# Kernel optimization log

Measured on AMD Instinct MI355X. Metric: run time of the kernel, lower is better.

## Reference

```python
import jax, jax.numpy as jnp
import numpy as np

B, G, A, C = 32, 2704, 3, 6
D, H, W = 1024, 52, 52
L, HID, K = 20, 512, 128


def setup_inputs() -> dict:
    key = jax.random.key(0)
    ks = jax.random.split(key, 7)
    return {
        "boxes": jax.random.normal(ks[0], (B, G, A, C), dtype=jnp.float32),
        "feature": jax.random.normal(ks[1], (B, D, H, W), dtype=jnp.float32),
        "text": jax.random.normal(ks[2], (B, L, HID), dtype=jnp.float32),
        "W_vs": jax.random.normal(ks[3], (D, HID), dtype=jnp.float32) * 0.02,
        "b_vs": jax.random.normal(ks[4], (HID,), dtype=jnp.float32) * 0.02,
        "W_tx": jax.random.normal(ks[5], (HID, HID), dtype=jnp.float32) * 0.02,
        "b_tx": jax.random.normal(ks[6], (HID,), dtype=jnp.float32) * 0.02,
        "select_num": K,
    }


def reference(boxes, feature, text, W_vs, b_vs, W_tx, b_tx, select_num):
    # objectness score: mean over anchors, channel 4  -> [B, G]
    score = jnp.mean(boxes, axis=2)[:, :, 4]
    _, idx = jax.lax.top_k(score, select_num)          # [B, K]
    # torch path builds a boolean mask then masked_select, which keeps
    # selected cells in grid order -> sort indices ascending
    idx = jnp.sort(idx, axis=1)

    # gather selected boxes: [B, K, A, C]
    sel_boxes = jnp.take_along_axis(boxes, idx[:, :, None, None], axis=1)

    b, d, h, w = feature.shape
    feat = feature.reshape(b, d, h * w).transpose(0, 2, 1)  # [B, G, D]
    sel_feat = jnp.take_along_axis(feat, idx[:, :, None], axis=1)  # [B, K, D]

    linear_feature = sel_feat @ W_vs + b_vs   # [B, K, HID]
    linear_text = text @ W_tx + b_tx          # [B, L, HID]

    # pack head inputs into a single array for baseline comparison
    out = jnp.concatenate([linear_feature, linear_text], axis=1)  # [B, K+L, HID]
    return out, sel_boxes
```

## Files before the change

kernel.cpp:

```cpp
#include <hip/hip_runtime.h>
#include <cstddef>

namespace {
constexpr int cB = 32;
constexpr int cG = 2704;
constexpr int cA = 3;
constexpr int cC = 6;
constexpr int cD = 1024;
constexpr int cL = 20;
constexpr int cH = 512;
constexpr int cK = 128;
constexpr int ROWS_OUT = cK + cL;
constexpr int CHUNK = (cG + 255) / 256;
}

using u16x8 = __attribute__((ext_vector_type(8))) unsigned short;
using f32x4 = __attribute__((ext_vector_type(4))) float;
using bf16x8 = __attribute__((ext_vector_type(8))) short;

static __device__ __forceinline__ unsigned short f2bf(float f) {
  unsigned u = __float_as_uint(f);
  unsigned rounding = 0x7fffu + ((u >> 16) & 1u);
  return (unsigned short)((u + rounding) >> 16);
}
static __device__ __forceinline__ unsigned packbf(float lo, float hi) {
  return (unsigned)f2bf(lo) | ((unsigned)f2bf(hi) << 16);
}

__global__ __launch_bounds__(256) void front_kernel(
    const float* __restrict__ boxes, const float* __restrict__ W_vs,
    const float* __restrict__ W_tx, const float* __restrict__ text,
    int* __restrict__ idx_out, float* __restrict__ out_boxes,
    unsigned short* __restrict__ Wt_vs, unsigned short* __restrict__ Wt_tx,
    unsigned short* __restrict__ text_bf) {
  __shared__ unsigned su[cG];
  __shared__ int hist[256];
  __shared__ int wsum[4];
  __shared__ int ssel[cK];
  __shared__ int s_rem;
  __shared__ unsigned s_prefix;
  __shared__ float tile[64][65];

  const int tid = threadIdx.x;
  const int lane = tid & 63;
  const int w4 = tid >> 6;

  if (blockIdx.x < cB) {
    const int b = blockIdx.x;
    for (int g = tid; g < cG; g += 256) {
      const float* p = boxes + ((size_t)(b * cG + g) * cA) * cC + 4;
      float s = (p[0] + p[cC] + p[2 * cC]) * (1.0f / 3.0f);
      unsigned bits = __float_as_uint(s);
      su[g] = (bits & 0x80000000u) ? ~bits : (bits | 0x80000000u);
    }
    __syncthreads();

    int remaining = cK;
    unsigned prefix = 0;
    for (int pass = 0; pass < 4; ++pass) {
      const int shift = 24 - 8 * pass;
      hist[tid] = 0;
      __syncthreads();
      for (int g = tid; g < cG; g += 256) {
        unsigned u = su[g];
        if ((pass == 0) || ((u >> (shift + 8)) == (prefix >> (shift + 8))))
          atomicAdd(&hist[(u >> shift) & 255], 1);
      }
      __syncthreads();
      int h = hist[tid];
      int x = h;
#pragma unroll
      for (int d = 1; d < 64; d <<= 1) {
        int n = __shfl_up(x, d);
        if (lane >= d) x += n;
      }
      if (lane == 63) wsum[w4] = x;
      __syncthreads();
      int off = 0, T = 0;
#pragma unroll
      for (int w = 0; w < 4; ++w) {
        int s = wsum[w];
        T += s;
        if (w < w4) off += s;
      }
      const int pincl = x + off;
      const int pexcl = pincl - h;
      const int target = T - remaining;
      if (target >= pexcl && target < pincl) {
        s_prefix = prefix | ((unsigned)tid << shift);
        s_rem = remaining - (T - pincl);
      }
      __syncthreads();
      remaining = s_rem;
      prefix = s_prefix;
    }

    const int g0 = tid * CHUNK;
    const int g1 = min(g0 + CHUNK, cG);
    int cgt = 0, ceq = 0;
    for (int g = g0; g < g1; ++g) {
      unsigned u = su[g];
      cgt += (u > prefix);
      ceq += (u == prefix);
    }
    int packed = (cgt << 16) | ceq;
    int x = packed;
#pragma unroll
    for (int d = 1; d < 64; d <<= 1) {
      int n = __shfl_up(x, d);
      if (lane >= d) x += n;
    }
    if (lane == 63) wsum[w4] = x;
    __syncthreads();
    int off = 0;
#pragma unroll
    for (int w = 0; w < 4; ++w)
      if (w < w4) off += wsum[w];
    const int excl = x + off - packed;
    int gt_before = excl >> 16;
    int eq_before = excl & 0xffff;

    for (int g = g0; g < g1; ++g) {
      unsigned u = su[g];
      if (u > prefix) {
        ssel[gt_before + min(eq_before, remaining)] = g;
        ++gt_before;
      } else if (u == prefix) {
        if (eq_before < remaining) ssel[gt_before + eq_before] = g;
        ++eq_before;
      }
    }
    __syncthreads();

    if (tid < cK) idx_out[b * cK + tid] = ssel[tid];
    for (int t2 = tid; t2 < cK * (cA * cC); t2 += 256) {
      const int k = t2 / 18;
      const int e = t2 - k * 18;
      out_boxes[(size_t)(b * cK + k) * 18 + e] =
          boxes[((size_t)(b * cG) + ssel[k]) * 18 + e];
    }
  } else {
    const int t = blockIdx.x - cB;
    if (t < 128) {
      const int k0 = (t >> 3) * 64, n0 = (t & 7) * 64;
      for (int i = tid; i < 1024; i += 256) {
        const int kk = i >> 4, c4 = (i & 15) * 4;
        const float4 v =
            *(const float4*)(W_vs + (size_t)(k0 + kk) * cH + n0 + c4);
        tile[kk][c4 + 0] = v.x;
        tile[kk][c4 + 1] = v.y;
        tile[kk][c4 + 2] = v.z;
        tile[kk][c4 + 3] = v.w;
      }
      __syncthreads();
      for (int j = tid; j < 2048; j += 256) {
        const int nn = j >> 5, p = j & 31;
        unsigned v = packbf(tile[2 * p][nn], tile[2 * p + 1][nn]);
        *(unsigned*)(Wt_vs + (size_t)(n0 + nn) * cD + k0 + 2 * p) = v;
      }
    } else if (t < 192) {
      const int t2 = t - 128;
      const int k0 = (t2 >> 3) * 64, n0 = (t2 & 7) * 64;
      for (int i = tid; i < 1024; i += 256) {
        const int kk = i >> 4, c4 = (i & 15) * 4;
        const float4 v =
            *(const float4*)(W_tx + (size_t)(k0 + kk) * cH + n0 + c4);
        tile[kk][c4 + 0] = v.x;
        tile[kk][c4 + 1] = v.y;
        tile[kk][c4 + 2] = v.z;
        tile[kk][c4 + 3] = v.w;
      }
      __syncthreads();
      for (int j = tid; j < 2048; j += 256) {
        const int nn = j >> 5, p = j & 31;
        unsigned v = packbf(tile[2 * p][nn], tile[2 * p + 1][nn]);
        *(unsigned*)(Wt_tx + (size_t)(n0 + nn) * cH + k0 + 2 * p) = v;
      }
    } else {
      const int t3 = t - 192;
      const size_t base = (size_t)t3 * 4096;
      for (int i = tid; i < 1024; i += 256) {
        const float4 v = *(const float4*)(text + base + (size_t)i * 4);
        uint2 pv;
        pv.x = packbf(v.x, v.y);
        pv.y = packbf(v.z, v.w);
        *(uint2*)(text_bf + base + (size_t)i * 4) = pv;
      }
    }
  }
}

__global__ __launch_bounds__(256) void gather_feat_kernel(
    const float* __restrict__ feature, const int* __restrict__ idx,
    unsigned short* __restrict__ selfeat) {
  const int kc = blockIdx.x, dc = blockIdx.y, b = blockIdx.z;
  const int lane = threadIdx.x & 63;
  const int grp = threadIdx.x >> 6;
  __shared__ int sidx[64];
  __shared__ float tile[64][65];
  if (threadIdx.x < 64) sidx[threadIdx.x] = idx[b * cK + kc * 64 + threadIdx.x];
  __syncthreads();

  const size_t fbase = (size_t)b * cD * cG + (size_t)(dc * 64) * cG;
  const int g = sidx[lane];
  for (int dd = grp; dd < 64; dd += 4) {
    tile[dd][lane] = feature[fbase + (size_t)dd * cG + g];
  }
  __syncthreads();

  const size_t obase = ((size_t)(b * cK + kc * 64)) * cD + dc * 64;
  for (int i = threadIdx.x; i < 64 * 32; i += 256) {
    const int kk = i >> 5;
    const int p = i & 31;
    unsigned v = packbf(tile[2 * p][kk], tile[2 * p + 1][kk]);
    *(unsigned*)(selfeat + obase + (size_t)kk * cD + 2 * p) = v;
  }
}

template <int KD>
__device__ __forceinline__ void mfma_gemm_body(
    const unsigned short* __restrict__ A, const unsigned short* __restrict__ Bt,
    const float* __restrict__ bias, float* __restrict__ out, int bm, int bn,
    int rpb, int row_off, unsigned short (*As)[128][40],
    unsigned short (*Bs)[128][40]) {
  constexpr int NT = KD / 32;
  const int tid = threadIdx.x;
  const int wid = tid >> 6, lane = tid & 63;
  const int wr = wid >> 1, wc = wid & 1;
  const int lr = lane & 15, lg = lane >> 4;

  const int srow = tid >> 2;
  const int sc = (tid & 3) * 8;

  const unsigned short* pA0 = A + (size_t)(bm * 128 + srow) * KD + sc;
  const unsigned short* pA1 = pA0 + (size_t)64 * KD;
  const unsigned short* pB0 = Bt + (size_t)(bn * 128 + srow) * KD + sc;
  const unsigned short* pB1 = pB0 + (size_t)64 * KD;

  f32x4 acc[4][4];
#pragma unroll
  for (int i = 0; i < 4; ++i)
#pragma unroll
    for (int j = 0; j < 4; ++j) acc[i][j] = {0.f, 0.f, 0.f, 0.f};

  u16x8 xa0, xa1, xb0, xb1;
  u16x8 ya0, ya1, yb0, yb1;

#define LOAD_X(kt)                           \
  xa0 = *(const u16x8*)(pA0 + (kt) * 32);    \
  xa1 = *(const u16x8*)(pA1 + (kt) * 32);    \
  xb0 = *(const u16x8*)(pB0 + (kt) * 32);    \
  xb1 = *(const u16x8*)(pB1 + (kt) * 32);
#define LOAD_Y(kt)                           \
  ya0 = *(const u16x8*)(pA0 + (kt) * 32);    \
  ya1 = *(const u16x8*)(pA1 + (kt) * 32);    \
  yb0 = *(const u16x8*)(pB0 + (kt) * 32);    \
  yb1 = *(const u16x8*)(pB1 + (kt) * 32);
#define STORE_X(buf)                         \
  *(u16x8*)&As[buf][srow][sc] = xa0;         \
  *(u16x8*)&As[buf][srow + 64][sc] = xa1;    \
  *(u16x8*)&Bs[buf][srow][sc] = xb0;         \
  *(u16x8*)&Bs[buf][srow + 64][sc] = xb1;
#define STORE_Y(buf)                         \
  *(u16x8*)&As[buf][srow][sc] = ya0;         \
  *(u16x8*)&As[buf][srow + 64][sc] = ya1;    \
  *(u16x8*)&Bs[buf][srow][sc] = yb0;         \
  *(u16x8*)&Bs[buf][srow + 64][sc] = yb1;
#define COMPUTE(buf)                                                        \
  {                                                                         \
    bf16x8 af[4], bfr[4];                                                   \
    _Pragma("unroll") for (int fr = 0; fr < 4; ++fr) af[fr] =               \
        *(const bf16x8*)&As[buf][wr * 64 + fr * 16 + lr][lg * 8];           \
    _Pragma("unroll") for (int fc = 0; fc < 4; ++fc) bfr[fc] =              \
        *(const bf16x8*)&Bs[buf][wc * 64 + fc * 16 + lr][lg * 8];           \
    _Pragma("unroll") for (int fr = 0; fr < 4; ++fr)                        \
        _Pragma("unroll") for (int fc = 0; fc < 4; ++fc) acc[fr][fc] =      \
            __builtin_amdgcn_mfma_f32_16x16x32_bf16(af[fr], bfr[fc],        \
                                                    acc[fr][fc], 0, 0, 0);  \
  }

  LOAD_X(0);
  LOAD_Y(1);
  STORE_X(0);
  __syncthreads();

  for (int t = 0; t < NT; t += 2) {
    if (t + 2 < NT) LOAD_X(t + 2);
    COMPUTE(0);
    STORE_Y(1);
    __syncthreads();
    if (t + 3 < NT) LOAD_Y(t + 3);
    COMPUTE(1);
    if (t + 2 < NT) STORE_X(0);
    __syncthreads();
  }
#undef LOAD_X
#undef LOAD_Y
#undef STORE_X
#undef STORE_Y
#undef COMPUTE

  float biasv[4];
#pragma unroll
  for (int fc = 0; fc < 4; ++fc)
    biasv[fc] = bias[bn * 128 + wc * 64 + fc * 16 + lr];

#pragma unroll
  for (int fr = 0; fr < 4; ++fr) {
#pragma unroll
    for (int fc = 0; fc < 4; ++fc) {
      const int col = bn * 128 + wc * 64 + fc * 16 + lr;
#pragma unroll
      for (int j = 0; j < 4; ++j) {
        const int row = bm * 128 + wr * 64 + fr * 16 + lg * 4 + j;
        const int bb = row / rpb;
        const int rr = row - bb * rpb;
        out[(size_t)bb * (ROWS_OUT * cH) + (size_t)(row_off + rr) * cH + col] =
            acc[fr][fc][j] + biasv[fc];
      }
    }
  }
}

__global__ __launch_bounds__(256) void gemms_kernel(
    const unsigned short* __restrict__ selfeat,
    const unsigned short* __restrict__ Wt_vs,
    const unsigned short* __restrict__ text_bf,
    const unsigned short* __restrict__ Wt_tx,
    const float* __restrict__ b_vs, const float* __restrict__ b_tx,
    float* __restrict__ out) {
  __shared__ unsigned short As[2][128][40];
  __shared__ unsigned short Bs[2][128][40];
  const int blk = blockIdx.x;
  if (blk < 128) {
    mfma_gemm_body<1024>(selfeat, Wt_vs, b_vs, out, blk >> 2, blk & 3, 128, 0,
                         As, Bs);
  } else {
    const int t = blk - 128;
    mfma_gemm_body<512>(text_bf, Wt_tx, b_tx, out, t >> 2, t & 3, cL, cK, As,
                        Bs);
  }
}

extern "C" void kernel_launch(void* const* d_in, const int* in_sizes, int n_in,
                              void* d_out, int out_size, void* d_ws,
                              size_t ws_size, hipStream_t stream) {
  const float* boxes = (const float*)d_in[0];
  const float* feature = (const float*)d_in[1];
  const float* text = (const float*)d_in[2];
  const float* W_vs = (const float*)d_in[3];
  const float* b_vs = (const float*)d_in[4];
  const float* W_tx = (const float*)d_in[5];
  const float* b_tx = (const float*)d_in[6];

  float* out = (float*)d_out;
  float* out_boxes = out + (size_t)cB * ROWS_OUT * cH;

  int* idx = (int*)d_ws;
  unsigned short* selfeat = (unsigned short*)((char*)d_ws + 16384);
  unsigned short* Wt_vs = (unsigned short*)((char*)d_ws + 8404992);
  unsigned short* Wt_tx = (unsigned short*)((char*)d_ws + 9453568);
  unsigned short* text_bf = (unsigned short*)((char*)d_ws + 9977856);

  front_kernel<<<cB + 272, 256, 0, stream>>>(boxes, W_vs, W_tx, text, idx,
                                             out_boxes, Wt_vs, Wt_tx, text_bf);

  {
    dim3 grid(cK / 64, cD / 64, cB);
    gather_feat_kernel<<<grid, 256, 0, stream>>>(feature, idx, selfeat);
  }

  gemms_kernel<<<148, 256, 0, stream>>>(selfeat, Wt_vs, text_bf, Wt_tx, b_vs,
                                        b_tx, out);
}
```

Baseline: 82.18 us.

## Halve gather tiles, widen GEMM blocks to 512 threads, swizzle block order

The gather kernel now covers 32 feature channels per block instead of 64, doubling the grid. Each thread issues 8 independent loads before writing to shared memory, and output is written as 8-byte packed stores. The GEMM kernel moves to 512 threads with 8 waves, each computing a 64x32 sub-tile, so the per-thread accumulators and staging loads are halved. The visual GEMM's block index is also remapped so that neighbouring blocks share B tiles. The goal is more parallelism and latency hiding on both kernels, at the cost of more blocks and redundant index loads in the gather.

```diff
diff --git a/kernel.cpp b/kernel.cpp
--- a/kernel.cpp
+++ b/kernel.cpp
@@ -193,27 +193,37 @@
 __global__ __launch_bounds__(256) void gather_feat_kernel(
     const float* __restrict__ feature, const int* __restrict__ idx,
     unsigned short* __restrict__ selfeat) {
-  const int kc = blockIdx.x, dc = blockIdx.y, b = blockIdx.z;
-  const int lane = threadIdx.x & 63;
-  const int grp = threadIdx.x >> 6;
+  const int kc = blockIdx.x;
+  const int dc = blockIdx.y;
+  const int b = blockIdx.z;
+  const int tid = threadIdx.x;
+  const int lane = tid & 63;
+  const int grp = tid >> 6;
   __shared__ int sidx[64];
-  __shared__ float tile[64][65];
-  if (threadIdx.x < 64) sidx[threadIdx.x] = idx[b * cK + kc * 64 + threadIdx.x];
+  __shared__ float tile[32][65];
+  if (tid < 64) sidx[tid] = idx[b * cK + kc * 64 + tid];
   __syncthreads();
 
-  const size_t fbase = (size_t)b * cD * cG + (size_t)(dc * 64) * cG;
   const int g = sidx[lane];
-  for (int dd = grp; dd < 64; dd += 4) {
-    tile[dd][lane] = feature[fbase + (size_t)dd * cG + g];
-  }
+  const float* fptr =
+      feature + (size_t)b * cD * cG + (size_t)(dc * 32 + grp * 8) * cG + g;
+  float f[8];
+#pragma unroll
+  for (int j = 0; j < 8; ++j) f[j] = fptr[(size_t)j * cG];
+#pragma unroll
+  for (int j = 0; j < 8; ++j) tile[grp * 8 + j][lane] = f[j];
   __syncthreads();
 
-  const size_t obase = ((size_t)(b * cK + kc * 64)) * cD + dc * 64;
-  for (int i = threadIdx.x; i < 64 * 32; i += 256) {
-    const int kk = i >> 5;
-    const int p = i & 31;
-    unsigned v = packbf(tile[2 * p][kk], tile[2 * p + 1][kk]);
-    *(unsigned*)(selfeat + obase + (size_t)kk * cD + 2 * p) = v;
+  const size_t obase = ((size_t)(b * cK + kc * 64)) * cD + dc * 32;
+#pragma unroll
+  for (int it = 0; it < 2; ++it) {
+    const int i = tid + it * 256;
+    const int kk = i >> 3;
+    const int q = i & 7;
+    uint2 pv;
+    pv.x = packbf(tile[4 * q + 0][kk], tile[4 * q + 1][kk]);
+    pv.y = packbf(tile[4 * q + 2][kk], tile[4 * q + 3][kk]);
+    *(uint2*)(selfeat + obase + (size_t)kk * cD + 4 * q) = pv;
   }
 }
 
@@ -226,55 +236,45 @@
   constexpr int NT = KD / 32;
   const int tid = threadIdx.x;
   const int wid = tid >> 6, lane = tid & 63;
-  const int wr = wid >> 1, wc = wid & 1;
+  const int wr = wid >> 2, wc = wid & 3;
   const int lr = lane & 15, lg = lane >> 4;
 
   const int srow = tid >> 2;
   const int sc = (tid & 3) * 8;
 
-  const unsigned short* pA0 = A + (size_t)(bm * 128 + srow) * KD + sc;
-  const unsigned short* pA1 = pA0 + (size_t)64 * KD;
-  const unsigned short* pB0 = Bt + (size_t)(bn * 128 + srow) * KD + sc;
-  const unsigned short* pB1 = pB0 + (size_t)64 * KD;
-
-  f32x4 acc[4][4];
+  const unsigned short* pA = A + (size_t)(bm * 128 + srow) * KD + sc;
+  const unsigned short* pB = Bt + (size_t)(bn * 128 + srow) * KD + sc;
+
+  f32x4 acc[4][2];
 #pragma unroll
   for (int i = 0; i < 4; ++i)
 #pragma unroll
-    for (int j = 0; j < 4; ++j) acc[i][j] = {0.f, 0.f, 0.f, 0.f};
-
-  u16x8 xa0, xa1, xb0, xb1;
-  u16x8 ya0, ya1, yb0, yb1;
-
-#define LOAD_X(kt)                           \
-  xa0 = *(const u16x8*)(pA0 + (kt) * 32);    \
-  xa1 = *(const u16x8*)(pA1 + (kt) * 32);    \
-  xb0 = *(const u16x8*)(pB0 + (kt) * 32);    \
-  xb1 = *(const u16x8*)(pB1 + (kt) * 32);
-#define LOAD_Y(kt)                           \
-  ya0 = *(const u16x8*)(pA0 + (kt) * 32);    \
-  ya1 = *(const u16x8*)(pA1 + (kt) * 32);    \
-  yb0 = *(const u16x8*)(pB0 + (kt) * 32);    \
-  yb1 = *(const u16x8*)(pB1 + (kt) * 32);
-#define STORE_X(buf)                         \
-  *(u16x8*)&As[buf][srow][sc] = xa0;         \
-  *(u16x8*)&As[buf][srow + 64][sc] = xa1;    \
-  *(u16x8*)&Bs[buf][srow][sc] = xb0;         \
-  *(u16x8*)&Bs[buf][srow + 64][sc] = xb1;
-#define STORE_Y(buf)                         \
-  *(u16x8*)&As[buf][srow][sc] = ya0;         \
-  *(u16x8*)&As[buf][srow + 64][sc] = ya1;    \
-  *(u16x8*)&Bs[buf][srow][sc] = yb0;         \
-  *(u16x8*)&Bs[buf][srow + 64][sc] = yb1;
+    for (int j = 0; j < 2; ++j) acc[i][j] = {0.f, 0.f, 0.f, 0.f};
+
+  u16x8 xa, xb;
+  u16x8 ya, yb;
+
+#define LOAD_X(kt)                      \
+  xa = *(const u16x8*)(pA + (kt) * 32); \
+  xb = *(const u16x8*)(pB + (kt) * 32);
+#define LOAD_Y(kt)                      \
+  ya = *(const u16x8*)(pA + (kt) * 32); \
+  yb = *(const u16x8*)(pB + (kt) * 32);
+#define STORE_X(buf)               \
+  *(u16x8*)&As[buf][srow][sc] = xa; \
+  *(u16x8*)&Bs[buf][srow][sc] = xb;
+#define STORE_Y(buf)               \
+  *(u16x8*)&As[buf][srow][sc] = ya; \
+  *(u16x8*)&Bs[buf][srow][sc] = yb;
 #define COMPUTE(buf)                                                        \
   {                                                                         \
-    bf16x8 af[4], bfr[4];                                                   \
+    bf16x8 af[4], bfr[2];                                                   \
     _Pragma("unroll") for (int fr = 0; fr < 4; ++fr) af[fr] =               \
         *(const bf16x8*)&As[buf][wr * 64 + fr * 16 + lr][lg * 8];           \
-    _Pragma("unroll") for (int fc = 0; fc < 4; ++fc) bfr[fc] =              \
-        *(const bf16x8*)&Bs[buf][wc * 64 + fc * 16 + lr][lg * 8];           \
+    _Pragma("unroll") for (int fc = 0; fc < 2; ++fc) bfr[fc] =              \
+        *(const bf16x8*)&Bs[buf][wc * 32 + fc * 16 + lr][lg * 8];           \
     _Pragma("unroll") for (int fr = 0; fr < 4; ++fr)                        \
-        _Pragma("unroll") for (int fc = 0; fc < 4; ++fc) acc[fr][fc] =      \
+        _Pragma("unroll") for (int fc = 0; fc < 2; ++fc) acc[fr][fc] =      \
             __builtin_amdgcn_mfma_f32_16x16x32_bf16(af[fr], bfr[fc],        \
                                                     acc[fr][fc], 0, 0, 0);  \
   }
@@ -300,16 +300,16 @@
 #undef STORE_Y
 #undef COMPUTE
 
-  float biasv[4];
-#pragma unroll
-  for (int fc = 0; fc < 4; ++fc)
-    biasv[fc] = bias[bn * 128 + wc * 64 + fc * 16 + lr];
+  float biasv[2];
+#pragma unroll
+  for (int fc = 0; fc < 2; ++fc)
+    biasv[fc] = bias[bn * 128 + wc * 32 + fc * 16 + lr];
 
 #pragma unroll
   for (int fr = 0; fr < 4; ++fr) {
 #pragma unroll
-    for (int fc = 0; fc < 4; ++fc) {
-      const int col = bn * 128 + wc * 64 + fc * 16 + lr;
+    for (int fc = 0; fc < 2; ++fc) {
+      const int col = bn * 128 + wc * 32 + fc * 16 + lr;
 #pragma unroll
       for (int j = 0; j < 4; ++j) {
         const int row = bm * 128 + wr * 64 + fr * 16 + lg * 4 + j;
@@ -322,19 +322,19 @@
   }
 }
 
-__global__ __launch_bounds__(256) void gemms_kernel(
+__global__ __launch_bounds__(512) void gemms_kernel(
     const unsigned short* __restrict__ selfeat,
     const unsigned short* __restrict__ Wt_vs,
     const unsigned short* __restrict__ text_bf,
-    const unsigned short* __restrict__ Wt_tx,
-    const float* __restrict__ b_vs, const float* __restrict__ b_tx,
-    float* __restrict__ out) {
+    const unsigned short* __restrict__ Wt_tx, const float* __restrict__ b_vs,
+    const float* __restrict__ b_tx, float* __restrict__ out) {
   __shared__ unsigned short As[2][128][40];
   __shared__ unsigned short Bs[2][128][40];
   const int blk = blockIdx.x;
   if (blk < 128) {
-    mfma_gemm_body<1024>(selfeat, Wt_vs, b_vs, out, blk >> 2, blk & 3, 128, 0,
-                         As, Bs);
+    const int w = ((blk & 7) << 4) | (blk >> 3);
+    mfma_gemm_body<1024>(selfeat, Wt_vs, b_vs, out, w >> 2, w & 3, 128, 0, As,
+                         Bs);
   } else {
     const int t = blk - 128;
     mfma_gemm_body<512>(text_bf, Wt_tx, b_tx, out, t >> 2, t & 3, cL, cK, As,
@@ -366,10 +366,10 @@
                                              out_boxes, Wt_vs, Wt_tx, text_bf);
 
   {
-    dim3 grid(cK / 64, cD / 64, cB);
+    dim3 grid(2, 32, 32);
     gather_feat_kernel<<<grid, 256, 0, stream>>>(feature, idx, selfeat);
   }
 
-  gemms_kernel<<<148, 256, 0, stream>>>(selfeat, Wt_vs, text_bf, Wt_tx, b_vs,
+  gemms_kernel<<<148, 512, 0, stream>>>(selfeat, Wt_vs, text_bf, Wt_tx, b_vs,
                                         b_tx, out);
 }
```

After: 81.56 us. Within noise of the previous version (-0.8%).
